# Optimization experiments

Measured on AMD Instinct MI355X. Metric: run time of the kernel, lower is better.

The kernel has to match this reference:

```python
import jax, jax.numpy as jnp
import numpy as np

B, L, E, H = 2, 2048, 512, 8
D = E // H  # head_dim = 64


def setup_inputs() -> dict:
    key = jax.random.key(0)
    ks = jax.random.split(key, 12)
    s = 0.02
    return {
        "values": jax.random.normal(ks[0], (B, L, E), jnp.float32),
        "keys": jax.random.normal(ks[1], (B, L, E), jnp.float32),
        "query": jax.random.normal(ks[2], (B, L, E), jnp.float32),
        "mask": jax.random.randint(ks[3], (B, 1, L, L), 0, 2, jnp.int32),
        "Wv": jax.random.normal(ks[4], (E, E), jnp.float32) * s,
        "bv": jax.random.normal(ks[5], (E,), jnp.float32) * s,
        "Wk": jax.random.normal(ks[6], (E, E), jnp.float32) * s,
        "bk": jax.random.normal(ks[7], (E,), jnp.float32) * s,
        "Wq": jax.random.normal(ks[8], (E, E), jnp.float32) * s,
        "bq": jax.random.normal(ks[9], (E,), jnp.float32) * s,
        "Wo": jax.random.normal(ks[10], (E, E), jnp.float32) * s,
        "bo": jax.random.normal(ks[11], (E,), jnp.float32) * s,
    }


def reference(values, keys, query, mask, Wv, bv, Wk, bk, Wq, bq, Wo, bo):
    b, lq = query.shape[0], query.shape[1]
    # torch Linear: y = x @ W.T + b
    v = (values @ Wv.T + bv).reshape(b, -1, H, D)
    k = (keys @ Wk.T + bk).reshape(b, -1, H, D)
    q = (query @ Wq.T + bq).reshape(b, lq, H, D)
    energy = jnp.einsum("bqhd,bkhd->bhqk", q, k)  # [B,H,Lq,Lk]
    # mask applied BEFORE the scale, as in the original
    energy = jnp.where(mask == 0, jnp.float32(-1e20), energy)
    # NOTE: scales by sqrt(embed_size), not sqrt(head_dim) (faithful)
    attn = jax.nn.softmax(energy / jnp.sqrt(jnp.float32(E)), axis=3)
    out = jnp.einsum("bhql,blhd->bqhd", attn, v).reshape(b, lq, E)
    return out @ Wo.T + bo
```

## Files before the change

kernel.cpp:

```cpp
#include <hip/hip_runtime.h>
#include <hip/hip_bf16.h>
#include <math.h>

#define BB 2
#define LL 2048
#define EE 512
#define HH 8
#define DD 64
#define MM (BB * LL)
#define LW (LL / 64)

typedef short bf16x8 __attribute__((ext_vector_type(8)));
typedef float f32x4 __attribute__((ext_vector_type(4)));

#define MFMA16(a, b, c) __builtin_amdgcn_mfma_f32_16x16x32_bf16((a), (b), (c), 0, 0, 0)

#if __has_builtin(__builtin_amdgcn_exp2f)
#define EXP2(x) __builtin_amdgcn_exp2f(x)
#else
#define EXP2(x) exp2f(x)
#endif

#define QSCALE 0.0637587146f

__device__ __forceinline__ void gl2lds16(const __hip_bfloat16* g, __hip_bfloat16* l) {
    __builtin_amdgcn_global_load_lds(
        (const __attribute__((address_space(1))) unsigned int*)(g),
        (__attribute__((address_space(3))) unsigned int*)(l),
        16, 0, 0);
}

__device__ __forceinline__ uint4 cvt8_bf16(const float4 a, const float4 b) {
    union { __hip_bfloat16 h[8]; uint4 u; } t;
    t.h[0] = __float2bfloat16(a.x); t.h[1] = __float2bfloat16(a.y);
    t.h[2] = __float2bfloat16(a.z); t.h[3] = __float2bfloat16(a.w);
    t.h[4] = __float2bfloat16(b.x); t.h[5] = __float2bfloat16(b.y);
    t.h[6] = __float2bfloat16(b.z); t.h[7] = __float2bfloat16(b.w);
    return t.u;
}

struct PrepArgs {
    const float* xsrc[3];
    __hip_bfloat16* xdst[3];
    const float* wsrc[4];
    __hip_bfloat16* wdst[4];
    const int* mask;
    unsigned long long* mbits;
};

__global__ __launch_bounds__(256) void prep(PrepArgs a) {
    const int blk = blockIdx.x;
    if (blk < 3072) {
        const int t = blk >> 10;
        const int i = ((blk & 1023) * 256 + threadIdx.x) * 8;
        const float* s = a.xsrc[t] + i;
        float4 f0 = *(const float4*)(s);
        float4 f1 = *(const float4*)(s + 4);
        *(uint4*)(a.xdst[t] + i) = cvt8_bf16(f0, f1);
    } else if (blk < 3584) {
        const int r = blk - 3072;
        const int t = r >> 7;
        const int i = ((r & 127) * 256 + threadIdx.x) * 8;
        const float* s = a.wsrc[t] + i;
        float4 f0 = *(const float4*)(s);
        float4 f1 = *(const float4*)(s + 4);
        *(uint4*)(a.wdst[t] + i) = cvt8_bf16(f0, f1);
    } else {
        const int mb = blk - 3584;
        #pragma unroll
        for (int r = 0; r < 16; ++r) {
            const size_t idx = ((size_t)mb * 16 + r) * 256 + threadIdx.x;
            const int m = a.mask[idx];
            const unsigned long long w = __ballot(m != 0);
            if ((threadIdx.x & 63) == 0) a.mbits[idx >> 6] = w;
        }
    }
}

struct QKVArgs {
    const __hip_bfloat16* X[3];
    const __hip_bfloat16* W[3];
    const float* bias[3];
    __hip_bfloat16* O[3];
};

__global__ __launch_bounds__(256) void gemm_qkv(QKVArgs p) {
    __shared__ __hip_bfloat16 As[2][2][64][32];
    __shared__ __hip_bfloat16 Bs[2][2][128][32];

    const int z = blockIdx.z;
    const __hip_bfloat16* __restrict__ X = p.X[z];
    const __hip_bfloat16* __restrict__ W = p.W[z];
    const float* __restrict__ bias = p.bias[z];
    __hip_bfloat16* __restrict__ O = p.O[z];

    const int tid = threadIdx.x;
    const int wave = tid >> 6, lane = tid & 63;
    const int l15 = lane & 15, quad = lane >> 4;
    const int wn = wave * 32;
    const int m0 = blockIdx.y * 64, n0 = blockIdx.x * 128;

    const int lr = lane >> 2;
    const int lc = (lane & 3) * 8;
    const __hip_bfloat16* Ax = X + (size_t)(m0 + wave * 16 + lr) * EE + lc;
    const __hip_bfloat16* Bx = W + (size_t)(n0 + wave * 32 + lr) * EE + lc;

    f32x4 acc[4][2] = {};

    #define STAGE_G(buf, k0)                                                   \
        gl2lds16(Ax + (k0),           &As[buf][0][wave * 16][0]);              \
        gl2lds16(Ax + (k0) + 32,      &As[buf][1][wave * 16][0]);              \
        gl2lds16(Bx + (k0),           &Bs[buf][0][wave * 32][0]);              \
        gl2lds16(Bx + (k0) + 32,      &Bs[buf][1][wave * 32][0]);              \
        gl2lds16(Bx + (k0) + 16 * EE,      &Bs[buf][0][wave * 32 + 16][0]);    \
        gl2lds16(Bx + (k0) + 16 * EE + 32, &Bs[buf][1][wave * 32 + 16][0]);

    STAGE_G(0, 0);
    __syncthreads();

    for (int kt = 0; kt < 8; ++kt) {
        const int cur = kt & 1;
        if (kt < 7) { STAGE_G(cur ^ 1, (kt + 1) * 64); }

        #pragma unroll
        for (int c = 0; c < 2; ++c) {
            bf16x8 af[4], bf2[2];
            #pragma unroll
            for (int i = 0; i < 4; ++i)
                af[i] = *(const bf16x8*)&As[cur][c][i * 16 + l15][quad * 8];
            #pragma unroll
            for (int j = 0; j < 2; ++j)
                bf2[j] = *(const bf16x8*)&Bs[cur][c][wn + j * 16 + l15][quad * 8];
            #pragma unroll
            for (int i = 0; i < 4; ++i)
                #pragma unroll
                for (int j = 0; j < 2; ++j)
                    acc[i][j] = MFMA16(af[i], bf2[j], acc[i][j]);
        }
        __syncthreads();
    }

    if (z == 2) {
        #pragma unroll
        for (int i = 0; i < 4; ++i)
            #pragma unroll
            for (int j = 0; j < 2; ++j) {
                const int n = n0 + wn + j * 16 + l15;
                const float bv = bias[n];
                const int h = n >> 6, d = n & 63;
                union { __hip_bfloat16 hh[4]; ushort4 v4; } pk;
                #pragma unroll
                for (int reg = 0; reg < 4; ++reg)
                    pk.hh[reg] = __float2bfloat16(acc[i][j][reg] + bv);
                const int m = m0 + i * 16 + quad * 4;
                const int bb = m >> 11, l = m & 2047;
                *(ushort4*)&O[(((size_t)bb * HH + h) * DD + d) * LL + l] = pk.v4;
            }
    } else {
        const float oscale = (z == 0) ? QSCALE : 1.0f;
        #pragma unroll
        for (int i = 0; i < 4; ++i)
            #pragma unroll
            for (int j = 0; j < 2; ++j) {
                const int n = n0 + wn + j * 16 + l15;
                const float bv = bias[n];
                #pragma unroll
                for (int reg = 0; reg < 4; ++reg) {
                    const int m = m0 + i * 16 + quad * 4 + reg;
                    O[(size_t)m * EE + n] = __float2bfloat16((acc[i][j][reg] + bv) * oscale);
                }
            }
    }
}

__global__ __launch_bounds__(256) void gemm_out(
    const __hip_bfloat16* __restrict__ X, const __hip_bfloat16* __restrict__ W,
    const float* __restrict__ bias, float* __restrict__ C) {
    __shared__ __hip_bfloat16 As[2][2][64][32];
    __shared__ __hip_bfloat16 Bs[2][2][128][32];

    const int tid = threadIdx.x;
    const int wave = tid >> 6, lane = tid & 63;
    const int l15 = lane & 15, quad = lane >> 4;
    const int wn = wave * 32;
    const int m0 = blockIdx.y * 64, n0 = blockIdx.x * 128;

    const int lr = lane >> 2;
    const int lc = (lane & 3) * 8;
    const __hip_bfloat16* Ax = X + (size_t)(m0 + wave * 16 + lr) * EE + lc;
    const __hip_bfloat16* Bx = W + (size_t)(n0 + wave * 32 + lr) * EE + lc;

    f32x4 acc[4][2] = {};

    STAGE_G(0, 0);
    __syncthreads();

    for (int kt = 0; kt < 8; ++kt) {
        const int cur = kt & 1;
        if (kt < 7) { STAGE_G(cur ^ 1, (kt + 1) * 64); }

        #pragma unroll
        for (int c = 0; c < 2; ++c) {
            bf16x8 af[4], bf2[2];
            #pragma unroll
            for (int i = 0; i < 4; ++i)
                af[i] = *(const bf16x8*)&As[cur][c][i * 16 + l15][quad * 8];
            #pragma unroll
            for (int j = 0; j < 2; ++j)
                bf2[j] = *(const bf16x8*)&Bs[cur][c][wn + j * 16 + l15][quad * 8];
            #pragma unroll
            for (int i = 0; i < 4; ++i)
                #pragma unroll
                for (int j = 0; j < 2; ++j)
                    acc[i][j] = MFMA16(af[i], bf2[j], acc[i][j]);
        }
        __syncthreads();
    }

    #pragma unroll
    for (int i = 0; i < 4; ++i)
        #pragma unroll
        for (int j = 0; j < 2; ++j) {
            const int n = n0 + wn + j * 16 + l15;
            const float bv = bias[n];
            #pragma unroll
            for (int reg = 0; reg < 4; ++reg) {
                const int m = m0 + i * 16 + quad * 4 + reg;
                C[(size_t)m * EE + n] = acc[i][j][reg] + bv;
            }
        }
}

__global__ __launch_bounds__(256) void attn_mfma(
    const __hip_bfloat16* __restrict__ Qb, const __hip_bfloat16* __restrict__ Kb,
    const __hip_bfloat16* __restrict__ vtg, const unsigned long long* __restrict__ mbits,
    __hip_bfloat16* __restrict__ Op) {
    __shared__ __hip_bfloat16 Ks[2][64][68];
    __shared__ __hip_bfloat16 Vs[2][64][68];
    __shared__ __hip_bfloat16 Ps[4][16][68];

    const int tid = threadIdx.x;
    const int wave = tid >> 6;
    const int lane = tid & 63;
    const int l15 = lane & 15;
    const int quad = lane >> 4;
    const int b = blockIdx.z;
    const int h = blockIdx.y;
    const int q0 = blockIdx.x * 64;
    const int myq = q0 + wave * 16 + l15;

    const int srow = tid >> 2;
    const int scg = (tid & 3) * 16;

    bf16x8 qf[2];
    {
        const __hip_bfloat16* qrow = Qb + ((size_t)b * LL + myq) * EE + h * DD;
        qf[0] = *(const bf16x8*)(qrow + quad * 8);
        qf[1] = *(const bf16x8*)(qrow + 32 + quad * 8);
    }

    const __hip_bfloat16* kbase = Kb + ((size_t)b * LL + srow) * EE + h * DD + scg;
    const __hip_bfloat16* vbase = vtg + (((size_t)b * HH + h) * DD + srow) * LL + scg;
    const unsigned long long* mrow = mbits + ((size_t)b * LL + myq) * LW;

    f32x4 o[4] = {};
    float lrun = 0.f;

    {
        uint4 k0a = *(const uint4*)(kbase);
        uint4 k0b = *(const uint4*)(kbase + 8);
        uint4 v0a = *(const uint4*)(vbase);
        uint4 v0b = *(const uint4*)(vbase + 8);
        *(uint4*)&Ks[0][srow][scg] = k0a;
        *(uint4*)&Ks[0][srow][scg + 8] = k0b;
        *(uint4*)&Vs[0][srow][scg] = v0a;
        *(uint4*)&Vs[0][srow][scg + 8] = v0b;
    }
    unsigned long long mw_cur = mrow[0];
    __syncthreads();

    for (int t = 0; t < LW; ++t) {
        const int cur = t & 1;
        const int nxt = cur ^ 1;
        const bool more = (t + 1) < LW;

        uint4 ka0, ka1, va0, va1;
        unsigned long long mw_n;
        if (more) {
            const __hip_bfloat16* kn = kbase + (size_t)(t + 1) * 64 * EE;
            const __hip_bfloat16* vn = vbase + (t + 1) * 64;
            ka0 = *(const uint4*)(kn);
            ka1 = *(const uint4*)(kn + 8);
            va0 = *(const uint4*)(vn);
            va1 = *(const uint4*)(vn + 8);
            mw_n = mrow[t + 1];
        }

        f32x4 st[4] = {};
        #pragma unroll
        for (int mt = 0; mt < 4; ++mt) {
            bf16x8 a0 = *(const bf16x8*)&Ks[cur][mt * 16 + l15][quad * 8];
            bf16x8 a1 = *(const bf16x8*)&Ks[cur][mt * 16 + l15][32 + quad * 8];
            st[mt] = MFMA16(a0, qf[0], st[mt]);
            st[mt] = MFMA16(a1, qf[1], st[mt]);
        }

        #pragma unroll
        for (int mt = 0; mt < 4; ++mt) {
            float p[4];
            #pragma unroll
            for (int reg = 0; reg < 4; ++reg) {
                const bool live = (mw_cur >> (mt * 16 + quad * 4 + reg)) & 1ull;
                const float e = EXP2(st[mt][reg]);
                p[reg] = live ? e : 0.f;
                lrun += p[reg];
            }
            union { __hip_bfloat162 h2[2]; ushort4 v; } pk;
            pk.h2[0] = __float22bfloat162_rn(make_float2(p[0], p[1]));
            pk.h2[1] = __float22bfloat162_rn(make_float2(p[2], p[3]));
            *(ushort4*)&Ps[wave][l15][mt * 16 + quad * 4] = pk.v;
        }

        bf16x8 pa0 = *(const bf16x8*)&Ps[wave][l15][quad * 8];
        bf16x8 pa1 = *(const bf16x8*)&Ps[wave][l15][32 + quad * 8];
        #pragma unroll
        for (int nt = 0; nt < 4; ++nt) {
            bf16x8 vb0 = *(const bf16x8*)&Vs[cur][nt * 16 + l15][quad * 8];
            bf16x8 vb1 = *(const bf16x8*)&Vs[cur][nt * 16 + l15][32 + quad * 8];
            o[nt] = MFMA16(pa0, vb0, o[nt]);
            o[nt] = MFMA16(pa1, vb1, o[nt]);
        }

        if (more) {
            *(uint4*)&Ks[nxt][srow][scg] = ka0;
            *(uint4*)&Ks[nxt][srow][scg + 8] = ka1;
            *(uint4*)&Vs[nxt][srow][scg] = va0;
            *(uint4*)&Vs[nxt][srow][scg + 8] = va1;
            mw_cur = mw_n;
        }
        __syncthreads();
    }

    lrun += __shfl_xor(lrun, 16);
    lrun += __shfl_xor(lrun, 32);
    const float linv = 1.f / lrun;
    float linvR[4];
    #pragma unroll
    for (int reg = 0; reg < 4; ++reg)
        linvR[reg] = __shfl(linv, quad * 4 + reg);

    __hip_bfloat16* Ob = Op + ((size_t)b * LL + q0 + wave * 16) * EE + h * DD;
    #pragma unroll
    for (int nt = 0; nt < 4; ++nt)
        #pragma unroll
        for (int reg = 0; reg < 4; ++reg) {
            const int qrow = quad * 4 + reg;
            Ob[(size_t)qrow * EE + nt * 16 + l15] =
                __float2bfloat16(o[nt][reg] * linvR[reg]);
        }
}

extern "C" void kernel_launch(void* const* d_in, const int* in_sizes, int n_in,
                              void* d_out, int out_size, void* d_ws, size_t ws_size,
                              hipStream_t stream) {
    const float* values = (const float*)d_in[0];
    const float* keys   = (const float*)d_in[1];
    const float* query  = (const float*)d_in[2];
    const int*   mask   = (const int*)d_in[3];
    const float* Wv = (const float*)d_in[4];
    const float* bv = (const float*)d_in[5];
    const float* Wk = (const float*)d_in[6];
    const float* bk = (const float*)d_in[7];
    const float* Wq = (const float*)d_in[8];
    const float* bq = (const float*)d_in[9];
    const float* Wo = (const float*)d_in[10];
    const float* bo = (const float*)d_in[11];
    float* out = (float*)d_out;

    const size_t XS = (size_t)MM * EE * 2;
    const size_t WS = (size_t)EE * EE * 2;
    char* w = (char*)d_ws;
    __hip_bfloat16* xq  = (__hip_bfloat16*)(w);
    __hip_bfloat16* xk  = (__hip_bfloat16*)(w + XS);
    __hip_bfloat16* xv  = (__hip_bfloat16*)(w + 2 * XS);
    __hip_bfloat16* qb  = (__hip_bfloat16*)(w + 3 * XS);
    __hip_bfloat16* kb  = (__hip_bfloat16*)(w + 4 * XS);
    __hip_bfloat16* vtg = (__hip_bfloat16*)(w + 5 * XS);
    __hip_bfloat16* aob = (__hip_bfloat16*)(w + 6 * XS);
    __hip_bfloat16* wqb = (__hip_bfloat16*)(w + 7 * XS);
    __hip_bfloat16* wkb = (__hip_bfloat16*)(w + 7 * XS + WS);
    __hip_bfloat16* wvb = (__hip_bfloat16*)(w + 7 * XS + 2 * WS);
    __hip_bfloat16* wob = (__hip_bfloat16*)(w + 7 * XS + 3 * WS);
    unsigned long long* mbits = (unsigned long long*)(w + 7 * XS + 4 * WS);

    PrepArgs pa;
    pa.xsrc[0] = query; pa.xsrc[1] = keys; pa.xsrc[2] = values;
    pa.xdst[0] = xq;    pa.xdst[1] = xk;   pa.xdst[2] = xv;
    pa.wsrc[0] = Wq; pa.wsrc[1] = Wk; pa.wsrc[2] = Wv; pa.wsrc[3] = Wo;
    pa.wdst[0] = wqb; pa.wdst[1] = wkb; pa.wdst[2] = wvb; pa.wdst[3] = wob;
    pa.mask = mask; pa.mbits = mbits;

    QKVArgs qa;
    qa.X[0] = xq;  qa.X[1] = xk;  qa.X[2] = xv;
    qa.W[0] = wqb; qa.W[1] = wkb; qa.W[2] = wvb;
    qa.bias[0] = bq; qa.bias[1] = bk; qa.bias[2] = bv;
    qa.O[0] = qb;  qa.O[1] = kb;  qa.O[2] = vtg;

    prep<<<5632, 256, 0, stream>>>(pa);
    gemm_qkv<<<dim3(EE / 128, MM / 64, 3), 256, 0, stream>>>(qa);
    attn_mfma<<<dim3(LL / 64, HH, BB), 256, 0, stream>>>(qb, kb, vtg, mbits, aob);
    gemm_out<<<dim3(EE / 128, MM / 64), 256, 0, stream>>>(aob, wob, bo, out);
}
```

Measured before the change: 184.1 us.

## Split attention KV range across two blocks with 32x32 MFMA and combine pass

Rewrites the attention kernel to use 32x32x16 MFMA tiles with 128-thread blocks. Each wave handles 32 queries, and P is kept in registers via permlane32 swaps instead of going through LDS. The key dimension is split into two halves processed by separate blocks, which write fp32 partial outputs and row sums. A new combine kernel merges the halves and normalizes. This aims to raise parallelism and cut LDS traffic, at the cost of extra fp32 partial writes and reads plus one more kernel launch. Op0 reuses the workspace region that held the converted inputs.

```diff
diff --git a/kernel.cpp b/kernel.cpp
--- a/kernel.cpp
+++ b/kernel.cpp
@@ -12,8 +12,10 @@
 
 typedef short bf16x8 __attribute__((ext_vector_type(8)));
 typedef float f32x4 __attribute__((ext_vector_type(4)));
+typedef float f32x16 __attribute__((ext_vector_type(16)));
 
 #define MFMA16(a, b, c) __builtin_amdgcn_mfma_f32_16x16x32_bf16((a), (b), (c), 0, 0, 0)
+#define MFMA32(a, b, c) __builtin_amdgcn_mfma_f32_32x32x16_bf16((a), (b), (c), 0, 0, 0)
 
 #if __has_builtin(__builtin_amdgcn_exp2f)
 #define EXP2(x) __builtin_amdgcn_exp2f(x)
@@ -231,133 +233,187 @@
         }
 }
 
-__global__ __launch_bounds__(256) void attn_mfma(
+__global__ __launch_bounds__(128, 2) void attn_mfma(
     const __hip_bfloat16* __restrict__ Qb, const __hip_bfloat16* __restrict__ Kb,
     const __hip_bfloat16* __restrict__ vtg, const unsigned long long* __restrict__ mbits,
-    __hip_bfloat16* __restrict__ Op) {
+    float* __restrict__ Op0, float* __restrict__ Op1, float* __restrict__ lp) {
     __shared__ __hip_bfloat16 Ks[2][64][68];
     __shared__ __hip_bfloat16 Vs[2][64][68];
-    __shared__ __hip_bfloat16 Ps[4][16][68];
 
     const int tid = threadIdx.x;
-    const int wave = tid >> 6;
-    const int lane = tid & 63;
-    const int l15 = lane & 15;
-    const int quad = lane >> 4;
-    const int b = blockIdx.z;
+    const int wave = tid >> 6, lane = tid & 63;
+    const int l31 = lane & 31, hi = lane >> 5;
+    const int b = blockIdx.z >> 1, sp = blockIdx.z & 1;
     const int h = blockIdx.y;
     const int q0 = blockIdx.x * 64;
-    const int myq = q0 + wave * 16 + l15;
-
-    const int srow = tid >> 2;
-    const int scg = (tid & 3) * 16;
-
-    bf16x8 qf[2];
+    const int qrow = q0 + wave * 32 + l31;
+
+    const int srow = tid >> 1, sc0 = (tid & 1) * 32;
+    const int NT = LW / 2;
+    const int t0 = sp * NT;
+
+    bf16x8 qf[4];
     {
-        const __hip_bfloat16* qrow = Qb + ((size_t)b * LL + myq) * EE + h * DD;
-        qf[0] = *(const bf16x8*)(qrow + quad * 8);
-        qf[1] = *(const bf16x8*)(qrow + 32 + quad * 8);
-    }
-
-    const __hip_bfloat16* kbase = Kb + ((size_t)b * LL + srow) * EE + h * DD + scg;
-    const __hip_bfloat16* vbase = vtg + (((size_t)b * HH + h) * DD + srow) * LL + scg;
-    const unsigned long long* mrow = mbits + ((size_t)b * LL + myq) * LW;
-
-    f32x4 o[4] = {};
+        const __hip_bfloat16* qr = Qb + ((size_t)b * LL + qrow) * EE + h * DD + hi * 8;
+        qf[0] = *(const bf16x8*)(qr);
+        qf[1] = *(const bf16x8*)(qr + 16);
+        qf[2] = *(const bf16x8*)(qr + 32);
+        qf[3] = *(const bf16x8*)(qr + 48);
+    }
+
+    const __hip_bfloat16* kbase =
+        Kb + ((size_t)b * LL + (size_t)t0 * 64 + srow) * EE + h * DD + sc0;
+    const __hip_bfloat16* vbase =
+        vtg + (((size_t)b * HH + h) * DD + srow) * LL + (size_t)t0 * 64 + sc0;
+    const unsigned long long* mrow = mbits + ((size_t)b * LL + qrow) * LW + t0;
+
+    f32x16 o0 = {}, o1 = {};
     float lrun = 0.f;
 
     {
-        uint4 k0a = *(const uint4*)(kbase);
-        uint4 k0b = *(const uint4*)(kbase + 8);
-        uint4 v0a = *(const uint4*)(vbase);
-        uint4 v0b = *(const uint4*)(vbase + 8);
-        *(uint4*)&Ks[0][srow][scg] = k0a;
-        *(uint4*)&Ks[0][srow][scg + 8] = k0b;
-        *(uint4*)&Vs[0][srow][scg] = v0a;
-        *(uint4*)&Vs[0][srow][scg + 8] = v0b;
+        uint4 k0 = *(const uint4*)(kbase);
+        uint4 k1 = *(const uint4*)(kbase + 8);
+        uint4 k2 = *(const uint4*)(kbase + 16);
+        uint4 k3 = *(const uint4*)(kbase + 24);
+        uint4 v0 = *(const uint4*)(vbase);
+        uint4 v1 = *(const uint4*)(vbase + 8);
+        uint4 v2 = *(const uint4*)(vbase + 16);
+        uint4 v3 = *(const uint4*)(vbase + 24);
+        *(uint4*)&Ks[0][srow][sc0] = k0;
+        *(uint4*)&Ks[0][srow][sc0 + 8] = k1;
+        *(uint4*)&Ks[0][srow][sc0 + 16] = k2;
+        *(uint4*)&Ks[0][srow][sc0 + 24] = k3;
+        *(uint4*)&Vs[0][srow][sc0] = v0;
+        *(uint4*)&Vs[0][srow][sc0 + 8] = v1;
+        *(uint4*)&Vs[0][srow][sc0 + 16] = v2;
+        *(uint4*)&Vs[0][srow][sc0 + 24] = v3;
     }
     unsigned long long mw_cur = mrow[0];
     __syncthreads();
 
-    for (int t = 0; t < LW; ++t) {
-        const int cur = t & 1;
-        const int nxt = cur ^ 1;
-        const bool more = (t + 1) < LW;
-
-        uint4 ka0, ka1, va0, va1;
+    for (int t = 0; t < NT; ++t) {
+        const int cur = t & 1, nxt = cur ^ 1;
+        const bool more = (t + 1) < NT;
+
+        uint4 kn0, kn1, kn2, kn3, vn0, vn1, vn2, vn3;
         unsigned long long mw_n;
         if (more) {
-            const __hip_bfloat16* kn = kbase + (size_t)(t + 1) * 64 * EE;
-            const __hip_bfloat16* vn = vbase + (t + 1) * 64;
-            ka0 = *(const uint4*)(kn);
-            ka1 = *(const uint4*)(kn + 8);
-            va0 = *(const uint4*)(vn);
-            va1 = *(const uint4*)(vn + 8);
+            const __hip_bfloat16* kp = kbase + (size_t)(t + 1) * 64 * EE;
+            const __hip_bfloat16* vp = vbase + (t + 1) * 64;
+            kn0 = *(const uint4*)(kp);      kn1 = *(const uint4*)(kp + 8);
+            kn2 = *(const uint4*)(kp + 16); kn3 = *(const uint4*)(kp + 24);
+            vn0 = *(const uint4*)(vp);      vn1 = *(const uint4*)(vp + 8);
+            vn2 = *(const uint4*)(vp + 16); vn3 = *(const uint4*)(vp + 24);
             mw_n = mrow[t + 1];
         }
 
-        f32x4 st[4] = {};
-        #pragma unroll
-        for (int mt = 0; mt < 4; ++mt) {
-            bf16x8 a0 = *(const bf16x8*)&Ks[cur][mt * 16 + l15][quad * 8];
-            bf16x8 a1 = *(const bf16x8*)&Ks[cur][mt * 16 + l15][32 + quad * 8];
-            st[mt] = MFMA16(a0, qf[0], st[mt]);
-            st[mt] = MFMA16(a1, qf[1], st[mt]);
-        }
-
-        #pragma unroll
-        for (int mt = 0; mt < 4; ++mt) {
-            float p[4];
-            #pragma unroll
-            for (int reg = 0; reg < 4; ++reg) {
-                const bool live = (mw_cur >> (mt * 16 + quad * 4 + reg)) & 1ull;
-                const float e = EXP2(st[mt][reg]);
-                p[reg] = live ? e : 0.f;
-                lrun += p[reg];
+        f32x16 st0 = {}, st1 = {};
+        #pragma unroll
+        for (int kk = 0; kk < 4; ++kk) {
+            bf16x8 kf0 = *(const bf16x8*)&Ks[cur][l31][kk * 16 + hi * 8];
+            bf16x8 kf1 = *(const bf16x8*)&Ks[cur][32 + l31][kk * 16 + hi * 8];
+            st0 = MFMA32(kf0, qf[kk], st0);
+            st1 = MFMA32(kf1, qf[kk], st1);
+        }
+
+        const unsigned long long msh = mw_cur >> (4 * hi);
+        const unsigned int m32a = (unsigned int)msh;
+        const unsigned int m32b = (unsigned int)(msh >> 32);
+        bf16x8 pa[4];
+        #pragma unroll
+        for (int kt = 0; kt < 2; ++kt) {
+            const f32x16 stv = kt ? st1 : st0;
+            const unsigned int mm = kt ? m32b : m32a;
+            float p[16];
+            #pragma unroll
+            for (int r = 0; r < 16; ++r) {
+                const int bit = (r & 3) + 8 * (r >> 2);
+                const float e = EXP2(stv[r]);
+                p[r] = ((mm >> bit) & 1u) ? e : 0.f;
             }
-            union { __hip_bfloat162 h2[2]; ushort4 v; } pk;
-            pk.h2[0] = __float22bfloat162_rn(make_float2(p[0], p[1]));
-            pk.h2[1] = __float22bfloat162_rn(make_float2(p[2], p[3]));
-            *(ushort4*)&Ps[wave][l15][mt * 16 + quad * 4] = pk.v;
-        }
-
-        bf16x8 pa0 = *(const bf16x8*)&Ps[wave][l15][quad * 8];
-        bf16x8 pa1 = *(const bf16x8*)&Ps[wave][l15][32 + quad * 8];
-        #pragma unroll
-        for (int nt = 0; nt < 4; ++nt) {
-            bf16x8 vb0 = *(const bf16x8*)&Vs[cur][nt * 16 + l15][quad * 8];
-            bf16x8 vb1 = *(const bf16x8*)&Vs[cur][nt * 16 + l15][32 + quad * 8];
-            o[nt] = MFMA16(pa0, vb0, o[nt]);
-            o[nt] = MFMA16(pa1, vb1, o[nt]);
+            lrun += (((p[0] + p[1]) + (p[2] + p[3])) + ((p[4] + p[5]) + (p[6] + p[7])))
+                  + (((p[8] + p[9]) + (p[10] + p[11])) + ((p[12] + p[13]) + (p[14] + p[15])));
+            unsigned int w[8];
+            #pragma unroll
+            for (int i = 0; i < 8; ++i) {
+                union { __hip_bfloat162 h2; unsigned int u; } cv;
+                cv.h2 = __float22bfloat162_rn(make_float2(p[2 * i], p[2 * i + 1]));
+                w[i] = cv.u;
+            }
+            asm volatile("v_permlane32_swap_b32 %0, %1" : "+v"(w[0]), "+v"(w[2]));
+            asm volatile("v_permlane32_swap_b32 %0, %1" : "+v"(w[1]), "+v"(w[3]));
+            asm volatile("v_permlane32_swap_b32 %0, %1" : "+v"(w[4]), "+v"(w[6]));
+            asm volatile("v_permlane32_swap_b32 %0, %1" : "+v"(w[5]), "+v"(w[7]));
+            union { unsigned int u[4]; bf16x8 v; } f0, f1;
+            f0.u[0] = w[0]; f0.u[1] = w[1]; f0.u[2] = w[2]; f0.u[3] = w[3];
+            f1.u[0] = w[4]; f1.u[1] = w[5]; f1.u[2] = w[6]; f1.u[3] = w[7];
+            pa[kt * 2] = f0.v;
+            pa[kt * 2 + 1] = f1.v;
+        }
+
+        #pragma unroll
+        for (int wd = 0; wd < 4; ++wd) {
+            bf16x8 vf0 = *(const bf16x8*)&Vs[cur][l31][wd * 16 + hi * 8];
+            bf16x8 vf1 = *(const bf16x8*)&Vs[cur][32 + l31][wd * 16 + hi * 8];
+            o0 = MFMA32(pa[wd], vf0, o0);
+            o1 = MFMA32(pa[wd], vf1, o1);
         }
 
         if (more) {
-            *(uint4*)&Ks[nxt][srow][scg] = ka0;
-            *(uint4*)&Ks[nxt][srow][scg + 8] = ka1;
-            *(uint4*)&Vs[nxt][srow][scg] = va0;
-            *(uint4*)&Vs[nxt][srow][scg + 8] = va1;
+            *(uint4*)&Ks[nxt][srow][sc0] = kn0;
+            *(uint4*)&Ks[nxt][srow][sc0 + 8] = kn1;
+            *(uint4*)&Ks[nxt][srow][sc0 + 16] = kn2;
+            *(uint4*)&Ks[nxt][srow][sc0 + 24] = kn3;
+            *(uint4*)&Vs[nxt][srow][sc0] = vn0;
+            *(uint4*)&Vs[nxt][srow][sc0 + 8] = vn1;
+            *(uint4*)&Vs[nxt][srow][sc0 + 16] = vn2;
+            *(uint4*)&Vs[nxt][srow][sc0 + 24] = vn3;
             mw_cur = mw_n;
         }
         __syncthreads();
     }
 
-    lrun += __shfl_xor(lrun, 16);
     lrun += __shfl_xor(lrun, 32);
-    const float linv = 1.f / lrun;
-    float linvR[4];
+    if (hi == 0)
+        lp[(((size_t)sp * BB + b) * HH + h) * LL + qrow] = lrun;
+
+    float* Opart = sp ? Op1 : Op0;
+    float* Ob = Opart + ((size_t)b * LL + q0 + wave * 32) * EE + h * DD;
     #pragma unroll
-    for (int reg = 0; reg < 4; ++reg)
-        linvR[reg] = __shfl(linv, quad * 4 + reg);
-
-    __hip_bfloat16* Ob = Op + ((size_t)b * LL + q0 + wave * 16) * EE + h * DD;
-    #pragma unroll
-    for (int nt = 0; nt < 4; ++nt)
-        #pragma unroll
-        for (int reg = 0; reg < 4; ++reg) {
-            const int qrow = quad * 4 + reg;
-            Ob[(size_t)qrow * EE + nt * 16 + l15] =
-                __float2bfloat16(o[nt][reg] * linvR[reg]);
-        }
+    for (int r = 0; r < 16; ++r) {
+        const int qr = (r & 3) + 8 * (r >> 2) + 4 * hi;
+        Ob[(size_t)qr * EE + l31] = o0[r];
+        Ob[(size_t)qr * EE + 32 + l31] = o1[r];
+    }
+}
+
+__global__ __launch_bounds__(256) void combine(
+    const float* __restrict__ Op0, const float* __restrict__ Op1,
+    const float* __restrict__ lp, __hip_bfloat16* __restrict__ aob) {
+    const int idx = blockIdx.x * 256 + threadIdx.x;
+    const int row = idx >> 6;
+    const int c0 = (idx & 63) * 8;
+    const int b = row >> 11, q = row & 2047;
+    const int h = c0 >> 6;
+    const float l0 = lp[((size_t)b * HH + h) * LL + q];
+    const float l1 = lp[(((size_t)BB + b) * HH + h) * LL + q];
+    const float linv = 1.f / (l0 + l1);
+    const float* p0 = Op0 + (size_t)row * EE + c0;
+    const float* p1 = Op1 + (size_t)row * EE + c0;
+    float4 a0 = *(const float4*)(p0);
+    float4 a1 = *(const float4*)(p0 + 4);
+    float4 b0 = *(const float4*)(p1);
+    float4 b1 = *(const float4*)(p1 + 4);
+    union { __hip_bfloat16 hh[8]; uint4 u; } pk;
+    pk.hh[0] = __float2bfloat16((a0.x + b0.x) * linv);
+    pk.hh[1] = __float2bfloat16((a0.y + b0.y) * linv);
+    pk.hh[2] = __float2bfloat16((a0.z + b0.z) * linv);
+    pk.hh[3] = __float2bfloat16((a0.w + b0.w) * linv);
+    pk.hh[4] = __float2bfloat16((a1.x + b1.x) * linv);
+    pk.hh[5] = __float2bfloat16((a1.y + b1.y) * linv);
+    pk.hh[6] = __float2bfloat16((a1.z + b1.z) * linv);
+    pk.hh[7] = __float2bfloat16((a1.w + b1.w) * linv);
+    *(uint4*)&aob[(size_t)row * EE + c0] = pk.u;
 }
 
 extern "C" void kernel_launch(void* const* d_in, const int* in_sizes, int n_in,
@@ -379,6 +435,8 @@
 
     const size_t XS = (size_t)MM * EE * 2;
     const size_t WS = (size_t)EE * EE * 2;
+    const size_t MBSZ = (size_t)BB * LL * LL / 8;
+    const size_t OPSZ = (size_t)BB * LL * EE * 4;
     char* w = (char*)d_ws;
     __hip_bfloat16* xq  = (__hip_bfloat16*)(w);
     __hip_bfloat16* xk  = (__hip_bfloat16*)(w + XS);
@@ -392,6 +450,9 @@
     __hip_bfloat16* wvb = (__hip_bfloat16*)(w + 7 * XS + 2 * WS);
     __hip_bfloat16* wob = (__hip_bfloat16*)(w + 7 * XS + 3 * WS);
     unsigned long long* mbits = (unsigned long long*)(w + 7 * XS + 4 * WS);
+    float* Op0 = (float*)(w);
+    float* Op1 = (float*)(w + 7 * XS + 4 * WS + MBSZ);
+    float* lp  = (float*)(w + 7 * XS + 4 * WS + MBSZ + OPSZ);
 
     PrepArgs pa;
     pa.xsrc[0] = query; pa.xsrc[1] = keys; pa.xsrc[2] = values;
@@ -408,6 +469,7 @@
 
     prep<<<5632, 256, 0, stream>>>(pa);
     gemm_qkv<<<dim3(EE / 128, MM / 64, 3), 256, 0, stream>>>(qa);
-    attn_mfma<<<dim3(LL / 64, HH, BB), 256, 0, stream>>>(qb, kb, vtg, mbits, aob);
+    attn_mfma<<<dim3(LL / 64, HH, BB * 2), 128, 0, stream>>>(qb, kb, vtg, mbits, Op0, Op1, lp);
+    combine<<<(MM * EE) / 2048, 256, 0, stream>>>(Op0, Op1, lp, aob);
     gemm_out<<<dim3(EE / 128, MM / 64), 256, 0, stream>>>(aob, wob, bo, out);
 }
```

Result: no change. 183.7 us (-0.2%).
